# Optimization experiments

Hardware: AMD Instinct MI355X
Metric: run time of the kernel (lower is better)

Reference implementation:

```python
import jax, jax.numpy as jnp
import numpy as np

INF, OUTF, BIT, GROUPSIZE = 4096, 11008, 4, 128
GROUPS = INF // GROUPSIZE  # 32
PACK = 32 // BIT           # 8 values per int32


def setup_inputs() -> dict:
    key = jax.random.key(0)
    k1, k2, k3, k4, k5 = jax.random.split(key, 5)
    x = jax.random.normal(k1, (2, 2048, INF), dtype=jnp.float32)
    # packed 4-bit weights: (INF*BIT/32, OUTF) int32
    qweight = jax.random.randint(k2, (INF * BIT // 32, OUTF), 0, 2147483647, dtype=jnp.int32)
    scales = jax.random.uniform(k3, (OUTF, GROUPS, 1), dtype=jnp.float32) * 0.01 + 0.001
    zeros = jax.random.uniform(k4, (OUTF, GROUPS, 1), dtype=jnp.float32) * 0.1
    bias = jax.random.normal(k5, (OUTF,), dtype=jnp.float32)
    return {"x": x, "qweight": qweight, "scales": scales, "zeros": zeros, "bias": bias}


def _dequant(qweight, scales, zeros):
    # unpack 8 nibbles per int32 row -> intweight (INF, OUTF)
    shifts = (BIT * jnp.arange(PACK, dtype=jnp.int32))[None, :, None]  # (1,8,1)
    nibbles = (qweight[:, None, :] >> shifts) & 0xF                    # (INF/8, 8, OUTF)
    wq = nibbles.reshape(INF, OUTF).astype(jnp.float32)
    # per-group dequant: W[k,n] = q*scale[n, k//gs] - zero[n, k//gs]
    s = scales[:, :, 0].T[:, None, :]  # (GROUPS, 1, OUTF)
    z = zeros[:, :, 0].T[:, None, :]
    w = wq.reshape(GROUPS, GROUPSIZE, OUTF) * s - z
    return w.reshape(INF, OUTF)


def reference(x, qweight, scales, zeros, bias):
    w = _dequant(qweight, scales, zeros)  # (INF, OUTF)
    # y = x @ W + bias  (matches y init to bias then vecquant4matmul accumulate)
    return jnp.einsum('bsk,kn->bsn', x, w) + bias
```

## Files before the change

### kernel.cpp

```cpp
#include <hip/hip_runtime.h>
#include <hip/hip_bf16.h>
#include <cstdint>
#include <cstddef>

#define K_DIM   4096
#define N_DIM   11008
#define M_DIM   4096
#define GROUPS  32
#define QROWS   512

typedef __bf16 bf16x8 __attribute__((ext_vector_type(8)));
typedef float  f32x4  __attribute__((ext_vector_type(4)));

__device__ __forceinline__ void async16(const void* g, void* lds) {
    __builtin_amdgcn_global_load_lds(
        (const __attribute__((address_space(1))) uint32_t*)g,
        (__attribute__((address_space(3))) uint32_t*)lds,
        16, 0, 0);
}

#define DQ_NN   64
#define DQ_KK   32
#define DQ_ROW  264
__global__ __launch_bounds__(256) void dequant_kernel(
        const uint32_t* __restrict__ qw,
        const float* __restrict__ scales,
        const float* __restrict__ zeros,
        __bf16* __restrict__ Wt) {
    __shared__ __align__(16) __bf16 T[DQ_NN * DQ_ROW];

    const int n0  = blockIdx.x * DQ_NN;
    const int kk0 = blockIdx.y * DQ_KK;
    const int tid = threadIdx.x;

#pragma unroll
    for (int it = 0; it < 8; ++it) {
        const int flat = it * 256 + tid;
        const int kk_l = flat >> 6;
        const int n_l  = flat & 63;
        const int kk   = kk0 + kk_l;
        const int n    = n0 + n_l;
        const uint32_t q = qw[(size_t)kk * N_DIM + n];
        const int g = kk >> 4;
        const float s = scales[(size_t)n * GROUPS + g];
        const float z = zeros[(size_t)n * GROUPS + g];
        bf16x8 w;
#pragma unroll
        for (int j = 0; j < 8; ++j) {
            float v = (float)((q >> (4 * j)) & 0xF) * s - z;
            w[j] = (__bf16)v;
        }
        *(bf16x8*)(&T[n_l * DQ_ROW + kk_l * 8]) = w;
    }
    __syncthreads();

#pragma unroll
    for (int it = 0; it < 8; ++it) {
        const int flat = it * 256 + tid;
        const int n_l    = flat >> 5;
        const int kchunk = flat & 31;
        bf16x8 v = *(const bf16x8*)(&T[n_l * DQ_ROW + kchunk * 8]);
        *(bf16x8*)(Wt + (size_t)(n0 + n_l) * K_DIM + (size_t)kk0 * 8 + kchunk * 8) = v;
    }
}

__global__ __launch_bounds__(256) void xconv_kernel(
        const float* __restrict__ x, __bf16* __restrict__ xb) {
    const size_t i = ((size_t)blockIdx.x * 256 + threadIdx.x) * 8;
    const float4* p = (const float4*)(x + i);
    float4 a = p[0];
    float4 b = p[1];
    bf16x8 o;
    o[0] = (__bf16)a.x; o[1] = (__bf16)a.y; o[2] = (__bf16)a.z; o[3] = (__bf16)a.w;
    o[4] = (__bf16)b.x; o[5] = (__bf16)b.y; o[6] = (__bf16)b.z; o[7] = (__bf16)b.w;
    *(bf16x8*)(xb + i) = o;
}

#define GN 86
#define GM 32
#define SN 16
__global__ __launch_bounds__(256, 4) void gemm_kernel(
        const __bf16* __restrict__ A,
        const __bf16* __restrict__ Bt,
        const float* __restrict__ bias,
        float* __restrict__ C) {
    __shared__ __align__(16) __bf16 As[128 * 32];
    __shared__ __align__(16) __bf16 Bs[128 * 32];

    const int tid  = threadIdx.x;
    const int wave = tid >> 6;
    const int lane = tid & 63;
    const int wm   = wave >> 1;
    const int wn   = wave & 1;
    const int quad = lane >> 4;
    const int l16  = lane & 15;

    const int bid = blockIdx.x;
    const int g   = bid >> 9;
    const int rem = bid & 511;
    int n_t, m_t;
    const int snw = (GN - g * SN) < SN ? (GN - g * SN) : SN;
    if (snw == SN) { n_t = g * SN + (rem & (SN - 1)); m_t = rem >> 4; }
    else           { n_t = g * SN + rem % snw;        m_t = rem / snw; }

    const int m0 = m_t * 128;
    const int n0 = n_t * 128;

    f32x4 acc[4][4] = {};

    const int c0 = wave * 128 + lane;
    const int c1 = c0 + 64;
    const __bf16* gA0 = A  + (size_t)(m0 + (c0 >> 2)) * K_DIM + (c0 & 3) * 8;
    const __bf16* gA1 = A  + (size_t)(m0 + (c1 >> 2)) * K_DIM + (c1 & 3) * 8;
    const __bf16* gB0 = Bt + (size_t)(n0 + (c0 >> 2)) * K_DIM + (c0 & 3) * 8;
    const __bf16* gB1 = Bt + (size_t)(n0 + (c1 >> 2)) * K_DIM + (c1 & 3) * 8;
    char* ldsA0 = (char*)As + (wave * 2 + 0) * 1024;
    char* ldsA1 = (char*)As + (wave * 2 + 1) * 1024;
    char* ldsB0 = (char*)Bs + (wave * 2 + 0) * 1024;
    char* ldsB1 = (char*)Bs + (wave * 2 + 1) * 1024;

    const __bf16* la = As + ((size_t)(wm * 64 + l16)) * 32 + quad * 8;
    const __bf16* lb = Bs + ((size_t)(wn * 64 + l16)) * 32 + quad * 8;

    for (int kt = 0; kt < K_DIM / 32; ++kt) {
        async16(gA0, ldsA0);
        async16(gA1, ldsA1);
        async16(gB0, ldsB0);
        async16(gB1, ldsB1);
        gA0 += 32; gA1 += 32; gB0 += 32; gB1 += 32;
        __syncthreads();

        bf16x8 af[4], bf[4];
#pragma unroll
        for (int i = 0; i < 4; ++i) af[i] = *(const bf16x8*)(la + i * 16 * 32);
#pragma unroll
        for (int i = 0; i < 4; ++i) bf[i] = *(const bf16x8*)(lb + i * 16 * 32);

#pragma unroll
        for (int i = 0; i < 4; ++i)
#pragma unroll
            for (int j = 0; j < 4; ++j)
                acc[i][j] = __builtin_amdgcn_mfma_f32_16x16x32_bf16(
                    af[i], bf[j], acc[i][j], 0, 0, 0);

        __syncthreads();
    }

#pragma unroll
    for (int j = 0; j < 4; ++j) {
        const int n = n0 + wn * 64 + j * 16 + l16;
        const float bv = bias[n];
#pragma unroll
        for (int i = 0; i < 4; ++i) {
            const int mb = m0 + wm * 64 + i * 16 + quad * 4;
#pragma unroll
            for (int r = 0; r < 4; ++r) {
                C[(size_t)(mb + r) * N_DIM + n] = acc[i][j][r] + bv;
            }
        }
    }
}

extern "C" void kernel_launch(void* const* d_in, const int* in_sizes, int n_in,
                              void* d_out, int out_size, void* d_ws, size_t ws_size,
                              hipStream_t stream) {
    const float*    x      = (const float*)d_in[0];
    const uint32_t* qw     = (const uint32_t*)d_in[1];
    const float*    scales = (const float*)d_in[2];
    const float*    zeros  = (const float*)d_in[3];
    const float*    bias   = (const float*)d_in[4];
    float*          out    = (float*)d_out;

    __bf16* Wt = (__bf16*)d_ws;
    __bf16* xb = (__bf16*)((char*)d_ws + (size_t)N_DIM * K_DIM * sizeof(__bf16));

    dim3 dq_grid(N_DIM / DQ_NN, QROWS / DQ_KK);
    dequant_kernel<<<dq_grid, 256, 0, stream>>>(qw, scales, zeros, Wt);
    xconv_kernel<<<(M_DIM * K_DIM) / (256 * 8), 256, 0, stream>>>(x, xb);

    gemm_kernel<<<GN * GM, 256, 0, stream>>>(xb, Wt, bias, out);
}
```

Before: 706.3 us.

## Merge dequant and x conversion into one launch; widen GEMM K tile to 64 with XOR swizzle

Folds the weight dequant and the fp32-to-bf16 activation conversion into a single prep kernel launch, with block ranges split by blockIdx, to save one launch and let the two kinds of work overlap. The GEMM K tile grows from 32 to 64, halving the number of K iterations and barriers. The shared-memory layout gains an XOR swizzle on 16-byte chunks to cut LDS bank conflicts on fragment reads. The larger tile doubles LDS use per block (32 KB), which may limit occupancy at 4 blocks per CU.

```diff
diff --git a/kernel.cpp b/kernel.cpp
--- a/kernel.cpp
+++ b/kernel.cpp
@@ -19,19 +19,40 @@
         16, 0, 0);
 }
 
-#define DQ_NN   64
-#define DQ_KK   32
-#define DQ_ROW  264
-__global__ __launch_bounds__(256) void dequant_kernel(
+#define DQ_NN     64
+#define DQ_KK     32
+#define DQ_ROW    264
+#define DQ_BLOCKS 2752
+#define XC_BLOCKS 2048
+
+__global__ __launch_bounds__(256) void prep_kernel(
         const uint32_t* __restrict__ qw,
         const float* __restrict__ scales,
         const float* __restrict__ zeros,
-        __bf16* __restrict__ Wt) {
+        __bf16* __restrict__ Wt,
+        const float* __restrict__ x,
+        __bf16* __restrict__ xb) {
     __shared__ __align__(16) __bf16 T[DQ_NN * DQ_ROW];
-
-    const int n0  = blockIdx.x * DQ_NN;
-    const int kk0 = blockIdx.y * DQ_KK;
     const int tid = threadIdx.x;
+
+    if (blockIdx.x >= DQ_BLOCKS) {
+        const int blk = blockIdx.x - DQ_BLOCKS;
+#pragma unroll
+        for (int u = 0; u < 4; ++u) {
+            const size_t i = (((size_t)blk * 4 + u) * 256 + tid) * 8;
+            const float4* p = (const float4*)(x + i);
+            float4 a = p[0];
+            float4 b = p[1];
+            bf16x8 o;
+            o[0] = (__bf16)a.x; o[1] = (__bf16)a.y; o[2] = (__bf16)a.z; o[3] = (__bf16)a.w;
+            o[4] = (__bf16)b.x; o[5] = (__bf16)b.y; o[6] = (__bf16)b.z; o[7] = (__bf16)b.w;
+            *(bf16x8*)(xb + i) = o;
+        }
+        return;
+    }
+
+    const int n0  = (blockIdx.x % 172) * DQ_NN;
+    const int kk0 = (blockIdx.x / 172) * DQ_KK;
 
 #pragma unroll
     for (int it = 0; it < 8; ++it) {
@@ -64,28 +85,18 @@
     }
 }
 
-__global__ __launch_bounds__(256) void xconv_kernel(
-        const float* __restrict__ x, __bf16* __restrict__ xb) {
-    const size_t i = ((size_t)blockIdx.x * 256 + threadIdx.x) * 8;
-    const float4* p = (const float4*)(x + i);
-    float4 a = p[0];
-    float4 b = p[1];
-    bf16x8 o;
-    o[0] = (__bf16)a.x; o[1] = (__bf16)a.y; o[2] = (__bf16)a.z; o[3] = (__bf16)a.w;
-    o[4] = (__bf16)b.x; o[5] = (__bf16)b.y; o[6] = (__bf16)b.z; o[7] = (__bf16)b.w;
-    *(bf16x8*)(xb + i) = o;
-}
-
 #define GN 86
 #define GM 32
 #define SN 16
+#define BK 64
+
 __global__ __launch_bounds__(256, 4) void gemm_kernel(
         const __bf16* __restrict__ A,
         const __bf16* __restrict__ Bt,
         const float* __restrict__ bias,
         float* __restrict__ C) {
-    __shared__ __align__(16) __bf16 As[128 * 32];
-    __shared__ __align__(16) __bf16 Bs[128 * 32];
+    __shared__ __align__(16) __bf16 As[128 * BK];
+    __shared__ __align__(16) __bf16 Bs[128 * BK];
 
     const int tid  = threadIdx.x;
     const int wave = tid >> 6;
@@ -108,40 +119,51 @@
 
     f32x4 acc[4][4] = {};
 
-    const int c0 = wave * 128 + lane;
-    const int c1 = c0 + 64;
-    const __bf16* gA0 = A  + (size_t)(m0 + (c0 >> 2)) * K_DIM + (c0 & 3) * 8;
-    const __bf16* gA1 = A  + (size_t)(m0 + (c1 >> 2)) * K_DIM + (c1 & 3) * 8;
-    const __bf16* gB0 = Bt + (size_t)(n0 + (c0 >> 2)) * K_DIM + (c0 & 3) * 8;
-    const __bf16* gB1 = Bt + (size_t)(n0 + (c1 >> 2)) * K_DIM + (c1 & 3) * 8;
-    char* ldsA0 = (char*)As + (wave * 2 + 0) * 1024;
-    char* ldsA1 = (char*)As + (wave * 2 + 1) * 1024;
-    char* ldsB0 = (char*)Bs + (wave * 2 + 0) * 1024;
-    char* ldsB1 = (char*)Bs + (wave * 2 + 1) * 1024;
-
-    const __bf16* la = As + ((size_t)(wm * 64 + l16)) * 32 + quad * 8;
-    const __bf16* lb = Bs + ((size_t)(wn * 64 + l16)) * 32 + quad * 8;
-
-    for (int kt = 0; kt < K_DIM / 32; ++kt) {
-        async16(gA0, ldsA0);
-        async16(gA1, ldsA1);
-        async16(gB0, ldsB0);
-        async16(gB1, ldsB1);
-        gA0 += 32; gA1 += 32; gB0 += 32; gB1 += 32;
+    const __bf16* gA[4];
+    const __bf16* gB[4];
+    char* ldsA[4];
+    char* ldsB[4];
+#pragma unroll
+    for (int i = 0; i < 4; ++i) {
+        const int c   = wave * 256 + i * 64 + lane;
+        const int row = c >> 3;
+        const int gk  = (c & 7) ^ (row & 7);
+        gA[i] = A  + (size_t)(m0 + row) * K_DIM + gk * 8;
+        gB[i] = Bt + (size_t)(n0 + row) * K_DIM + gk * 8;
+        ldsA[i] = (char*)As + (wave * 4 + i) * 1024;
+        ldsB[i] = (char*)Bs + (wave * 4 + i) * 1024;
+    }
+
+    const int xr = l16 & 7;
+    const __bf16* la = As + (size_t)(wm * 64 + l16) * BK;
+    const __bf16* lb = Bs + (size_t)(wn * 64 + l16) * BK;
+
+    for (int kt = 0; kt < K_DIM / BK; ++kt) {
+#pragma unroll
+        for (int i = 0; i < 4; ++i) async16(gA[i], ldsA[i]);
+#pragma unroll
+        for (int i = 0; i < 4; ++i) async16(gB[i], ldsB[i]);
+#pragma unroll
+        for (int i = 0; i < 4; ++i) { gA[i] += BK; gB[i] += BK; }
         __syncthreads();
 
-        bf16x8 af[4], bf[4];
-#pragma unroll
-        for (int i = 0; i < 4; ++i) af[i] = *(const bf16x8*)(la + i * 16 * 32);
-#pragma unroll
-        for (int i = 0; i < 4; ++i) bf[i] = *(const bf16x8*)(lb + i * 16 * 32);
-
-#pragma unroll
-        for (int i = 0; i < 4; ++i)
-#pragma unroll
-            for (int j = 0; j < 4; ++j)
-                acc[i][j] = __builtin_amdgcn_mfma_f32_16x16x32_bf16(
-                    af[i], bf[j], acc[i][j], 0, 0, 0);
+#pragma unroll
+        for (int s = 0; s < 2; ++s) {
+            bf16x8 af[4], bf[4];
+#pragma unroll
+            for (int i = 0; i < 4; ++i)
+                af[i] = *(const bf16x8*)(la + i * 16 * BK + (((s * 4 + quad) ^ xr) * 8));
+#pragma unroll
+            for (int i = 0; i < 4; ++i)
+                bf[i] = *(const bf16x8*)(lb + i * 16 * BK + (((s * 4 + quad) ^ xr) * 8));
+
+#pragma unroll
+            for (int i = 0; i < 4; ++i)
+#pragma unroll
+                for (int j = 0; j < 4; ++j)
+                    acc[i][j] = __builtin_amdgcn_mfma_f32_16x16x32_bf16(
+                        af[i], bf[j], acc[i][j], 0, 0, 0);
+        }
 
         __syncthreads();
     }
@@ -174,9 +196,7 @@
     __bf16* Wt = (__bf16*)d_ws;
     __bf16* xb = (__bf16*)((char*)d_ws + (size_t)N_DIM * K_DIM * sizeof(__bf16));
 
-    dim3 dq_grid(N_DIM / DQ_NN, QROWS / DQ_KK);
-    dequant_kernel<<<dq_grid, 256, 0, stream>>>(qw, scales, zeros, Wt);
-    xconv_kernel<<<(M_DIM * K_DIM) / (256 * 8), 256, 0, stream>>>(x, xb);
+    prep_kernel<<<DQ_BLOCKS + XC_BLOCKS, 256, 0, stream>>>(qw, scales, zeros, Wt, x, xb);
 
     gemm_kernel<<<GN * GM, 256, 0, stream>>>(xb, Wt, bias, out);
 }
```

Result: slower. 782.5 us (+10.8%).
